# Performance work log

Measured on AMD Instinct MI355X. Metric: run time of the kernel, lower is better.

The kernel has to match this reference:

```python
import jax, jax.numpy as jnp
import numpy as np

N_NODES = 100_000
N_EDGES = 1_600_000
N_GRAPHS = 1024
IN_CH = 5
EPS_BN = 1e-5


def _p(key, shape, scale=0.1):
    return scale * jax.random.normal(key, shape, dtype=jnp.float32)


def setup_inputs() -> dict:
    key = jax.random.key(0)
    ks = jax.random.split(key, 24)
    x = jax.random.normal(ks[0], (N_NODES, IN_CH), dtype=jnp.float32)
    edge_index = jax.random.randint(ks[1], (2, N_EDGES), 0, N_NODES, dtype=jnp.int64)
    batch = jnp.sort(jax.random.randint(ks[2], (N_NODES,), 0, N_GRAPHS, dtype=jnp.int64))
    return {
        "x": x, "edge_index": edge_index, "batch": batch,
        "W1": _p(ks[3], (IN_CH, 128)), "a1_src": _p(ks[4], (4, 32)), "a1_dst": _p(ks[5], (4, 32)), "b1": jnp.zeros((128,), jnp.float32),
        "g1": jnp.ones((128,), jnp.float32), "be1": jnp.zeros((128,), jnp.float32),
        "W2": _p(ks[6], (128, 128)), "a2_src": _p(ks[7], (4, 32)), "a2_dst": _p(ks[8], (4, 32)), "b2": jnp.zeros((128,), jnp.float32),
        "g2": jnp.ones((128,), jnp.float32), "be2": jnp.zeros((128,), jnp.float32),
        # conv3: 128 -> 64, 1 head, mean (concat=False)
        "W3": _p(ks[9], (128, 64)), "a3_src": _p(ks[10], (1, 64)), "a3_dst": _p(ks[11], (1, 64)), "b3": jnp.zeros((64,), jnp.float32),
        # classifier Linear(128,64) -> ELU -> Linear(64,1)
        "fc1_w": _p(ks[12], (128, 64)), "fc1_b": jnp.zeros((64,), jnp.float32),
        "fc2_w": _p(ks[13], (64, 1)), "fc2_b": jnp.zeros((1,), jnp.float32),
    }


def _gat_conv(x, src, dst, W, a_src, a_dst, bias, heads, out_ch, concat):
    """PyG GATConv (negative_slope=0.2, self-loops already appended, eval-mode dropout)."""
    n = x.shape[0]
    h = (x @ W).reshape(n, heads, out_ch)                      # [N,H,C]
    al_s = jnp.sum(h * a_src, axis=-1)                         # [N,H]
    al_d = jnp.sum(h * a_dst, axis=-1)                         # [N,H]
    e = jax.nn.leaky_relu(al_s[src] + al_d[dst], 0.2)          # [E,H]
    m = jax.lax.stop_gradient(jax.ops.segment_max(e, dst, num_segments=n))
    p = jnp.exp(e - m[dst])
    s = jax.ops.segment_sum(p, dst, num_segments=n)
    alpha = p / (s[dst] + 1e-16)                               # segment softmax over in-edges of dst
    out = jax.ops.segment_sum(h[src] * alpha[:, :, None], dst, num_segments=n)  # [N,H,C]
    out = out.reshape(n, heads * out_ch) if concat else out.mean(axis=1)
    return out + bias


def _bn(x, g, b):
    mu = x.mean(axis=0)
    var = x.var(axis=0)
    return (x - mu) * jax.lax.rsqrt(var + EPS_BN) * g + b


def reference(x, edge_index, batch,
              W1, a1_src, a1_dst, b1, g1, be1,
              W2, a2_src, a2_dst, b2, g2, be2,
              W3, a3_src, a3_dst, b3,
              fc1_w, fc1_b, fc2_w, fc2_b):
    n = x.shape[0]
    # PyG GATConv default add_self_loops=True
    loops = jnp.arange(n, dtype=edge_index.dtype)
    src = jnp.concatenate([edge_index[0], loops])
    dst = jnp.concatenate([edge_index[1], loops])

    h = jax.nn.elu(_bn(_gat_conv(x, src, dst, W1, a1_src, a1_dst, b1, 4, 32, True), g1, be1))
    h = jax.nn.elu(_bn(_gat_conv(h, src, dst, W2, a2_src, a2_dst, b2, 4, 32, True), g2, be2))
    h = jax.nn.elu(_gat_conv(h, src, dst, W3, a3_src, a3_dst, b3, 1, 64, False))  # [N,64]

    counts = jax.ops.segment_sum(jnp.ones((n,), h.dtype), batch, num_segments=N_GRAPHS)
    mean_p = jax.ops.segment_sum(h, batch, num_segments=N_GRAPHS) / jnp.maximum(counts, 1.0)[:, None]
    max_p = jax.ops.segment_max(h, batch, num_segments=N_GRAPHS)
    max_p = jnp.where(counts[:, None] > 0, max_p, 0.0)
    hg = jnp.concatenate([mean_p, max_p], axis=1)              # [B,128]

    z = jax.nn.elu(hg @ fc1_w + fc1_b)
    return (z @ fc2_w + fc2_b).squeeze(-1)                     # [B]
```

## Files before the change

### kernel.cpp

```cpp
#include <hip/hip_runtime.h>
#include <hip/hip_bf16.h>


#define BSHIFT 7
#define BCAP 4096
#define SCH 32

typedef __attribute__((ext_vector_type(8))) short short8;
typedef __attribute__((ext_vector_type(4))) float f32x4;

__device__ __forceinline__ float leaky02(float e) { return e > 0.f ? e : 0.2f * e; }

__device__ __forceinline__ unsigned short bf16u(float x) {
    __hip_bfloat16 b = __float2bfloat16(x);
    return *(unsigned short*)&b;
}
__device__ __forceinline__ unsigned pack_bf2(float a, float b) {
    return (unsigned)bf16u(a) | ((unsigned)bf16u(b) << 16);
}
__device__ __forceinline__ float bf_lo(unsigned u) { return __uint_as_float(u << 16); }
__device__ __forceinline__ float bf_hi(unsigned u) { return __uint_as_float(u & 0xffff0000u); }

__global__ __launch_bounds__(256) void k_bhist(const int* __restrict__ dst,
                                               int* __restrict__ bcount, int E, int nb) {
    __shared__ int hist[1024];
    for (int i = threadIdx.x; i < nb; i += 256) hist[i] = 0;
    __syncthreads();
    for (int i = blockIdx.x * blockDim.x + threadIdx.x; i < E; i += gridDim.x * blockDim.x)
        atomicAdd(&hist[dst[i] >> BSHIFT], 1);
    __syncthreads();
    for (int i = threadIdx.x; i < nb; i += 256) {
        int c = hist[i];
        if (c) atomicAdd(&bcount[i], c);
    }
}

__global__ __launch_bounds__(1024) void k_bscan(const int* __restrict__ bcount,
                                                int* __restrict__ bucketPtr,
                                                int* __restrict__ cursor,
                                                int* __restrict__ rowPtr, int nb, int N) {
    __shared__ int sh[1024];
    int tid = threadIdx.x;
    int v = (tid < nb) ? bcount[tid] : 0;
    sh[tid] = v;
    __syncthreads();
#pragma unroll
    for (int off = 1; off < 1024; off <<= 1) {
        int t = (tid >= off) ? sh[tid - off] : 0;
        __syncthreads();
        sh[tid] += t;
        __syncthreads();
    }
    if (tid < nb) {
        int ex = sh[tid] - v;
        bucketPtr[tid] = ex;
        cursor[tid] = ex;
    }
    if (tid == nb - 1) {
        bucketPtr[nb] = sh[tid];
        rowPtr[N] = sh[tid];
    }
}

__global__ __launch_bounds__(256) void k_bscatter(const int* __restrict__ src,
                                                  const int* __restrict__ dst,
                                                  int* __restrict__ cursor,
                                                  uint2* __restrict__ ebuf, int E, int nb) {
    __shared__ int hist[1024];
    __shared__ int baseArr[1024];
    int tid = threadIdx.x;
    int chunk0 = blockIdx.x * (256 * SCH);
    for (int i = tid; i < nb; i += 256) hist[i] = 0;
    __syncthreads();
    int rank[SCH];
#pragma unroll
    for (int it = 0; it < SCH; it++) {
        int e = chunk0 + it * 256 + tid;
        rank[it] = (e < E) ? atomicAdd(&hist[dst[e] >> BSHIFT], 1) : 0;
    }
    __syncthreads();
    for (int b = tid; b < nb; b += 256) {
        int c = hist[b];
        baseArr[b] = c ? atomicAdd(&cursor[b], c) : 0;
    }
    __syncthreads();
#pragma unroll
    for (int it = 0; it < SCH; it++) {
        int e = chunk0 + it * 256 + tid;
        if (e < E) {
            int d = dst[e];
            int pos = baseArr[d >> BSHIFT] + rank[it];
            ebuf[pos] = make_uint2((unsigned)d, (unsigned)src[e]);
        }
    }
}

__global__ __launch_bounds__(256) void k_bsort(const uint2* __restrict__ ebuf,
                                               const int* __restrict__ bucketPtr,
                                               int* __restrict__ rowPtr,
                                               int* __restrict__ colv, int N) {
    int b = blockIdx.x;
    int base = bucketPtr[b], end = bucketPtr[b + 1];
    int count = end - base;
    int tid = threadIdx.x;
    __shared__ int hist[128], scanin[128], hist2[128];
    __shared__ int lrank[BCAP];
    __shared__ int lsrc[BCAP];
    if (tid < 128) { hist[tid] = 0; hist2[tid] = 0; }
    __syncthreads();
    bool staged = (count <= BCAP);
    for (int i = tid; i < count; i += 256) {
        uint2 p = ebuf[base + i];
        int local = p.x & 127;
        int r = atomicAdd(&hist[local], 1);
        if (staged) lrank[i] = (r << 7) | local;
    }
    __syncthreads();
    if (tid < 128) scanin[tid] = hist[tid];
    __syncthreads();
#pragma unroll
    for (int off = 1; off < 128; off <<= 1) {
        int v = 0;
        if (tid < 128 && tid >= off) v = scanin[tid - off];
        __syncthreads();
        if (tid < 128) scanin[tid] += v;
        __syncthreads();
    }
    int nodeBase = b << BSHIFT;
    if (tid < 128) {
        int n = nodeBase + tid;
        if (n < N) rowPtr[n] = base + scanin[tid] - hist[tid];
    }
    __syncthreads();
    if (staged) {
        for (int i = tid; i < count; i += 256) {
            uint2 p = ebuf[base + i];
            int lr = lrank[i];
            int local = lr & 127;
            int pos = (scanin[local] - hist[local]) + (lr >> 7);
            lsrc[pos] = (int)p.y;
        }
        __syncthreads();
        for (int i = tid; i < count; i += 256) colv[base + i] = lsrc[i];
    } else {
        for (int i = tid; i < count; i += 256) {
            uint2 p = ebuf[base + i];
            int local = p.x & 127;
            int r = atomicAdd(&hist2[local], 1);
            colv[base + (scanin[local] - hist[local]) + r] = (int)p.y;
        }
    }
}

__global__ __launch_bounds__(256) void k_l1(const float* __restrict__ x, const float* __restrict__ W,
                                            const float* __restrict__ asrc, const float* __restrict__ adst,
                                            unsigned* __restrict__ hb, float* __restrict__ als,
                                            float* __restrict__ ald, int N) {
    int w = (blockIdx.x * blockDim.x + threadIdx.x) >> 6;
    if (w >= N) return;
    int lane = threadIdx.x & 63;
    float xv[5];
#pragma unroll
    for (int k = 0; k < 5; k++) xv[k] = x[(size_t)w * 5 + k];
    int c0 = 2 * lane;
    float h0 = 0.f, h1 = 0.f;
#pragma unroll
    for (int k = 0; k < 5; k++) {
        float2 wv = ((const float2*)(W + k * 128))[lane];
        h0 += xv[k] * wv.x;
        h1 += xv[k] * wv.y;
    }
    hb[(size_t)w * 64 + lane] = pack_bf2(h0, h1);
    float s = h0 * asrc[c0] + h1 * asrc[c0 + 1];
    float d = h0 * adst[c0] + h1 * adst[c0 + 1];
#pragma unroll
    for (int off = 1; off <= 8; off <<= 1) { s += __shfl_xor(s, off); d += __shfl_xor(d, off); }
    if ((lane & 15) == 0) {
        int g = lane >> 4;
        als[(size_t)w * 4 + g] = s;
        ald[(size_t)w * 4 + g] = d;
    }
}

__global__ __launch_bounds__(256) void k_agg128(const unsigned* __restrict__ h,
                                                const float* __restrict__ als, const float* __restrict__ ald,
                                                const int* __restrict__ rowPtr, const int* __restrict__ colv,
                                                const float* __restrict__ bias,
                                                float* __restrict__ out, int N) {
    int w = (blockIdx.x * blockDim.x + threadIdx.x) >> 6;
    if (w >= N) return;
    int lane = threadIdx.x & 63;
    int grp = lane >> 4;
    int l16 = lane & 15;
    int head = l16 >> 2;
    float aldn = ald[(size_t)w * 4 + head];
    float acc[8] = {};
    float dsum = 0.f;

    auto edge = [&](int s) {
        float a = als[(size_t)s * 4 + head];
        float wt = __expf(leaky02(a + aldn));
        uint4 u = *(const uint4*)&h[(size_t)s * 64 + l16 * 4];
        acc[0] += wt * bf_lo(u.x); acc[1] += wt * bf_hi(u.x);
        acc[2] += wt * bf_lo(u.y); acc[3] += wt * bf_hi(u.y);
        acc[4] += wt * bf_lo(u.z); acc[5] += wt * bf_hi(u.z);
        acc[6] += wt * bf_lo(u.w); acc[7] += wt * bf_hi(u.w);
        dsum += wt;
    };

    if (grp == 0) edge(w);
    int beg = rowPtr[w], end = rowPtr[w + 1];
    int p = beg + grp;
    for (; p + 12 < end; p += 16) {
        int s0 = colv[p], s1 = colv[p + 4], s2 = colv[p + 8], s3 = colv[p + 12];
        float a0 = als[(size_t)s0 * 4 + head];
        float a1 = als[(size_t)s1 * 4 + head];
        float a2 = als[(size_t)s2 * 4 + head];
        float a3 = als[(size_t)s3 * 4 + head];
        uint4 u0 = *(const uint4*)&h[(size_t)s0 * 64 + l16 * 4];
        uint4 u1 = *(const uint4*)&h[(size_t)s1 * 64 + l16 * 4];
        uint4 u2 = *(const uint4*)&h[(size_t)s2 * 64 + l16 * 4];
        uint4 u3 = *(const uint4*)&h[(size_t)s3 * 64 + l16 * 4];
        float w0 = __expf(leaky02(a0 + aldn));
        float w1 = __expf(leaky02(a1 + aldn));
        float w2 = __expf(leaky02(a2 + aldn));
        float w3 = __expf(leaky02(a3 + aldn));
        acc[0] += w0 * bf_lo(u0.x) + w1 * bf_lo(u1.x) + w2 * bf_lo(u2.x) + w3 * bf_lo(u3.x);
        acc[1] += w0 * bf_hi(u0.x) + w1 * bf_hi(u1.x) + w2 * bf_hi(u2.x) + w3 * bf_hi(u3.x);
        acc[2] += w0 * bf_lo(u0.y) + w1 * bf_lo(u1.y) + w2 * bf_lo(u2.y) + w3 * bf_lo(u3.y);
        acc[3] += w0 * bf_hi(u0.y) + w1 * bf_hi(u1.y) + w2 * bf_hi(u2.y) + w3 * bf_hi(u3.y);
        acc[4] += w0 * bf_lo(u0.z) + w1 * bf_lo(u1.z) + w2 * bf_lo(u2.z) + w3 * bf_lo(u3.z);
        acc[5] += w0 * bf_hi(u0.z) + w1 * bf_hi(u1.z) + w2 * bf_hi(u2.z) + w3 * bf_hi(u3.z);
        acc[6] += w0 * bf_lo(u0.w) + w1 * bf_lo(u1.w) + w2 * bf_lo(u2.w) + w3 * bf_lo(u3.w);
        acc[7] += w0 * bf_hi(u0.w) + w1 * bf_hi(u1.w) + w2 * bf_hi(u2.w) + w3 * bf_hi(u3.w);
        dsum += w0 + w1 + w2 + w3;
    }
    for (; p < end; p += 4) edge(colv[p]);

#pragma unroll
    for (int i = 0; i < 8; i++) {
        acc[i] += __shfl_xor(acc[i], 16);
        acc[i] += __shfl_xor(acc[i], 32);
    }
    dsum += __shfl_xor(dsum, 16);
    dsum += __shfl_xor(dsum, 32);

    if (grp == 0) {
        float inv = 1.f / (dsum + 1e-16f);
        const float4* b4 = (const float4*)(bias + 8 * l16);
        float4 bv0 = b4[0], bv1 = b4[1];
        float4 o0, o1;
        o0.x = acc[0] * inv + bv0.x; o0.y = acc[1] * inv + bv0.y;
        o0.z = acc[2] * inv + bv0.z; o0.w = acc[3] * inv + bv0.w;
        o1.x = acc[4] * inv + bv1.x; o1.y = acc[5] * inv + bv1.y;
        o1.z = acc[6] * inv + bv1.z; o1.w = acc[7] * inv + bv1.w;
        float4* op = (float4*)(out + (size_t)w * 128 + 8 * l16);
        op[0] = o0;
        op[1] = o1;
    }
}

__global__ __launch_bounds__(256) void k_agg64(const unsigned* __restrict__ h,
                                               const float* __restrict__ als, const float* __restrict__ ald,
                                               const int* __restrict__ rowPtr, const int* __restrict__ colv,
                                               const float* __restrict__ bias,
                                               float* __restrict__ out, int N) {
    int w = (blockIdx.x * blockDim.x + threadIdx.x) >> 6;
    if (w >= N) return;
    int lane = threadIdx.x & 63;
    int grp = lane >> 3;
    int l8 = lane & 7;
    float aldn = ald[w];
    float acc[8] = {};
    float dsum = 0.f;

    auto edge = [&](int s) {
        float wt = __expf(leaky02(als[s] + aldn));
        uint4 u = *(const uint4*)&h[(size_t)s * 32 + l8 * 4];
        acc[0] += wt * bf_lo(u.x); acc[1] += wt * bf_hi(u.x);
        acc[2] += wt * bf_lo(u.y); acc[3] += wt * bf_hi(u.y);
        acc[4] += wt * bf_lo(u.z); acc[5] += wt * bf_hi(u.z);
        acc[6] += wt * bf_lo(u.w); acc[7] += wt * bf_hi(u.w);
        dsum += wt;
    };

    if (grp == 0) edge(w);
    int beg = rowPtr[w], end = rowPtr[w + 1];
    int p = beg + grp;
    for (; p + 8 < end; p += 16) {
        int s0 = colv[p], s1 = colv[p + 8];
        float a0 = als[s0], a1 = als[s1];
        uint4 u0 = *(const uint4*)&h[(size_t)s0 * 32 + l8 * 4];
        uint4 u1 = *(const uint4*)&h[(size_t)s1 * 32 + l8 * 4];
        float w0 = __expf(leaky02(a0 + aldn));
        float w1 = __expf(leaky02(a1 + aldn));
        acc[0] += w0 * bf_lo(u0.x) + w1 * bf_lo(u1.x);
        acc[1] += w0 * bf_hi(u0.x) + w1 * bf_hi(u1.x);
        acc[2] += w0 * bf_lo(u0.y) + w1 * bf_lo(u1.y);
        acc[3] += w0 * bf_hi(u0.y) + w1 * bf_hi(u1.y);
        acc[4] += w0 * bf_lo(u0.z) + w1 * bf_lo(u1.z);
        acc[5] += w0 * bf_hi(u0.z) + w1 * bf_hi(u1.z);
        acc[6] += w0 * bf_lo(u0.w) + w1 * bf_lo(u1.w);
        acc[7] += w0 * bf_hi(u0.w) + w1 * bf_hi(u1.w);
        dsum += w0 + w1;
    }
    if (p < end) edge(colv[p]);

#pragma unroll
    for (int i = 0; i < 8; i++) {
        acc[i] += __shfl_xor(acc[i], 8);
        acc[i] += __shfl_xor(acc[i], 16);
        acc[i] += __shfl_xor(acc[i], 32);
    }
    dsum += __shfl_xor(dsum, 8);
    dsum += __shfl_xor(dsum, 16);
    dsum += __shfl_xor(dsum, 32);

    if (grp == 0) {
        float inv = 1.f / (dsum + 1e-16f);
        const float4* b4 = (const float4*)(bias + 8 * l8);
        float4 bv0 = b4[0], bv1 = b4[1];
        float v[8];
#pragma unroll
        for (int i = 0; i < 8; i++) v[i] = acc[i] * inv;
        v[0] += bv0.x; v[1] += bv0.y; v[2] += bv0.z; v[3] += bv0.w;
        v[4] += bv1.x; v[5] += bv1.y; v[6] += bv1.z; v[7] += bv1.w;
#pragma unroll
        for (int i = 0; i < 8; i++) v[i] = v[i] > 0.f ? v[i] : expm1f(v[i]);
        float4* op = (float4*)(out + (size_t)w * 64 + 8 * l8);
        op[0] = make_float4(v[0], v[1], v[2], v[3]);
        op[1] = make_float4(v[4], v[5], v[6], v[7]);
    }
}

__global__ __launch_bounds__(256) void k_bnstats(const float* __restrict__ x,
                                                 float* __restrict__ stats, int N) {
    int tid = threadIdx.x;
    int c = tid & 127;
    int half = tid >> 7;
    float s = 0.f, q = 0.f;
    for (int r = blockIdx.x * 2 + half; r < N; r += gridDim.x * 2) {
        float v = x[(size_t)r * 128 + c];
        s += v;
        q += v * v;
    }
    __shared__ float ls[256], lq[256];
    ls[tid] = s; lq[tid] = q;
    __syncthreads();
    if (tid < 128) {
        atomicAdd(&stats[c], ls[tid] + ls[tid + 128]);
        atomicAdd(&stats[128 + c], lq[tid] + lq[tid + 128]);
    }
}

template <int BN>
__global__ __launch_bounds__(256) void k_gemm_mfma(
        const float* __restrict__ A, const float* __restrict__ W,
        const float* __restrict__ stats, const float* __restrict__ g,
        const float* __restrict__ be,
        unsigned* __restrict__ hb, float* __restrict__ als, float* __restrict__ ald,
        const float* __restrict__ asrc, const float* __restrict__ adst,
        int M, float invN) {
    constexpr int NT = BN / 16;
    __shared__ unsigned short Wt[BN][136];
    __shared__ unsigned short At[64][136];
    __shared__ float sc[128], sh[128];
    const int tid = threadIdx.x;
    const int wave = tid >> 6, lane = tid & 63;
    const int quad = lane >> 4, l16 = lane & 15;
    const int r0 = blockIdx.x * 64;

    if (tid < 128) {
        float mean = stats[tid] * invN;
        float var = stats[128 + tid] * invN - mean * mean;
        float s = rsqrtf(var + 1e-5f) * g[tid];
        sc[tid] = s;
        sh[tid] = be[tid] - mean * s;
    }
    for (int i = tid; i < 128 * (BN / 4); i += 256) {
        int k = i / (BN / 4);
        int n4 = (i % (BN / 4)) * 4;
        float4 v = *(const float4*)(W + (size_t)k * BN + n4);
        Wt[n4 + 0][k] = bf16u(v.x);
        Wt[n4 + 1][k] = bf16u(v.y);
        Wt[n4 + 2][k] = bf16u(v.z);
        Wt[n4 + 3][k] = bf16u(v.w);
    }
    __syncthreads();
    for (int i = tid; i < 64 * 32; i += 256) {
        int row = i >> 5;
        int c4 = (i & 31) << 2;
        int r = r0 + row;
        float4 v = make_float4(0.f, 0.f, 0.f, 0.f);
        if (r < M) v = *(const float4*)(A + (size_t)r * 128 + c4);
        float t0 = v.x * sc[c4 + 0] + sh[c4 + 0];
        float t1 = v.y * sc[c4 + 1] + sh[c4 + 1];
        float t2 = v.z * sc[c4 + 2] + sh[c4 + 2];
        float t3 = v.w * sc[c4 + 3] + sh[c4 + 3];
        t0 = t0 > 0.f ? t0 : expm1f(t0);
        t1 = t1 > 0.f ? t1 : expm1f(t1);
        t2 = t2 > 0.f ? t2 : expm1f(t2);
        t3 = t3 > 0.f ? t3 : expm1f(t3);
        unsigned u0 = (unsigned)bf16u(t0) | ((unsigned)bf16u(t1) << 16);
        unsigned u1 = (unsigned)bf16u(t2) | ((unsigned)bf16u(t3) << 16);
        *(uint2*)&At[row][c4] = make_uint2(u0, u1);
    }
    __syncthreads();

    short8 afr[4];
#pragma unroll
    for (int ks = 0; ks < 4; ks++)
        afr[ks] = *(const short8*)&At[wave * 16 + l16][ks * 32 + quad * 8];
    f32x4 acc[NT];
#pragma unroll
    for (int nt = 0; nt < NT; nt++) acc[nt] = (f32x4){0.f, 0.f, 0.f, 0.f};
#pragma unroll
    for (int ks = 0; ks < 4; ks++) {
#pragma unroll
        for (int nt = 0; nt < NT; nt++) {
            short8 bfrag = *(const short8*)&Wt[nt * 16 + l16][ks * 32 + quad * 8];
            acc[nt] = __builtin_amdgcn_mfma_f32_16x16x32_bf16(afr[ks], bfrag, acc[nt], 0, 0, 0);
        }
    }

    float as_[NT], ad_[NT];
#pragma unroll
    for (int nt = 0; nt < NT; nt++) {
        as_[nt] = asrc[nt * 16 + l16];
        ad_[nt] = adst[nt * 16 + l16];
    }

#pragma unroll
    for (int r = 0; r < 4; r++) {
        int gr = r0 + wave * 16 + quad * 4 + r;
        if constexpr (BN == 128) {
            float sv[4] = {0.f, 0.f, 0.f, 0.f}, dv[4] = {0.f, 0.f, 0.f, 0.f};
#pragma unroll
            for (int nt = 0; nt < NT; nt++) {
                float v = acc[nt][r];
                sv[nt >> 1] += v * as_[nt];
                dv[nt >> 1] += v * ad_[nt];
            }
#pragma unroll
            for (int hd = 0; hd < 4; hd++) {
                float s = sv[hd], d = dv[hd];
                s += __shfl_xor(s, 1); s += __shfl_xor(s, 2);
                s += __shfl_xor(s, 4); s += __shfl_xor(s, 8);
                d += __shfl_xor(d, 1); d += __shfl_xor(d, 2);
                d += __shfl_xor(d, 4); d += __shfl_xor(d, 8);
                if (l16 == 0 && gr < M) {
                    als[(size_t)gr * 4 + hd] = s;
                    ald[(size_t)gr * 4 + hd] = d;
                }
            }
        } else {
            float s = 0.f, d = 0.f;
#pragma unroll
            for (int nt = 0; nt < NT; nt++) {
                float v = acc[nt][r];
                s += v * as_[nt];
                d += v * ad_[nt];
            }
            s += __shfl_xor(s, 1); s += __shfl_xor(s, 2);
            s += __shfl_xor(s, 4); s += __shfl_xor(s, 8);
            d += __shfl_xor(d, 1); d += __shfl_xor(d, 2);
            d += __shfl_xor(d, 4); d += __shfl_xor(d, 8);
            if (l16 == 0 && gr < M) { als[gr] = s; ald[gr] = d; }
        }
    }
#pragma unroll
    for (int nt = 0; nt < NT; nt++) {
#pragma unroll
        for (int r = 0; r < 4; r++) {
            float v = acc[nt][r];
            float o = __shfl_xor(v, 1);
            if ((lane & 1) == 0) {
                int gr = r0 + wave * 16 + quad * 4 + r;
                if (gr < M)
                    hb[(size_t)gr * (BN / 2) + nt * 8 + (l16 >> 1)] = pack_bf2(v, o);
            }
        }
    }
}

__global__ __launch_bounds__(64) void k_pool(const float* __restrict__ h, const int* __restrict__ batch,
                                             const float* __restrict__ fc1w, const float* __restrict__ fc1b,
                                             const float* __restrict__ fc2w, const float* __restrict__ fc2b,
                                             float* __restrict__ out, int N) {
    int g = blockIdx.x;
    int lane = threadIdx.x;
    int lo, hi;
    {
        int a = 0, b = N;
        while (a < b) { int m = (a + b) >> 1; if (batch[m] < g) a = m + 1; else b = m; }
        lo = a;
    }
    {
        int a = lo, b = N;
        while (a < b) { int m = (a + b) >> 1; if (batch[m] < g + 1) a = m + 1; else b = m; }
        hi = a;
    }
    float sum = 0.f, mx = -3.4e38f;
    for (int r = lo; r < hi; r++) {
        float v = h[(size_t)r * 64 + lane];
        sum += v;
        mx = fmaxf(mx, v);
    }
    int cnt = hi - lo;
    float mean = sum / fmaxf((float)cnt, 1.f);
    if (cnt == 0) mx = 0.f;
    __shared__ float hg[128];
    hg[lane] = mean;
    hg[64 + lane] = mx;
    __syncthreads();
    float z = fc1b[lane];
    for (int k = 0; k < 128; k++) z += hg[k] * fc1w[k * 64 + lane];
    z = z > 0.f ? z : expm1f(z);
    float o = z * fc2w[lane];
#pragma unroll
    for (int off = 32; off >= 1; off >>= 1) o += __shfl_down(o, off);
    if (lane == 0) out[g] = o + fc2b[0];
}

extern "C" void kernel_launch(void* const* d_in, const int* in_sizes, int n_in,
                              void* d_out, int out_size, void* d_ws, size_t ws_size,
                              hipStream_t stream) {
    const float* x = (const float*)d_in[0];
    const int* ei = (const int*)d_in[1];
    const int* batch = (const int*)d_in[2];
    const float* W1 = (const float*)d_in[3];
    const float* a1s = (const float*)d_in[4];
    const float* a1d = (const float*)d_in[5];
    const float* b1 = (const float*)d_in[6];
    const float* g1 = (const float*)d_in[7];
    const float* be1 = (const float*)d_in[8];
    const float* W2 = (const float*)d_in[9];
    const float* a2s = (const float*)d_in[10];
    const float* a2d = (const float*)d_in[11];
    const float* b2 = (const float*)d_in[12];
    const float* g2 = (const float*)d_in[13];
    const float* be2 = (const float*)d_in[14];
    const float* W3 = (const float*)d_in[15];
    const float* a3s = (const float*)d_in[16];
    const float* a3d = (const float*)d_in[17];
    const float* b3 = (const float*)d_in[18];
    const float* fc1w = (const float*)d_in[19];
    const float* fc1b = (const float*)d_in[20];
    const float* fc2w = (const float*)d_in[21];
    const float* fc2b = (const float*)d_in[22];

    const int N = in_sizes[2];
    const int E = in_sizes[1] / 2;
    const int NG = out_size;
    const int* src = ei;
    const int* dst = ei + E;
    const int nb = (N + 127) >> BSHIFT;

    char* ws = (char*)d_ws;
    size_t off = 0;
    auto alloc = [&](size_t bytes) -> void* {
        void* p = ws + off;
        off += (bytes + 255) / 256 * 256;
        return p;
    };
    float* bufA = (float*)alloc((size_t)N * 128 * 4);
    unsigned* hb = (unsigned*)alloc((size_t)N * 64 * 4);
    float* h3 = (float*)alloc((size_t)N * 64 * 4);
    int* colArr = (int*)alloc((size_t)E * 4);
    int* rowPtr = (int*)alloc((size_t)(N + 1) * 4);
    int* bcount = (int*)alloc((size_t)nb * 4);
    int* bucketPtr = (int*)alloc((size_t)(nb + 1) * 4);
    int* cursor = (int*)alloc((size_t)nb * 4);
    float* als = (float*)alloc((size_t)N * 4 * 4);
    float* ald = (float*)alloc((size_t)N * 4 * 4);
    float* stats = (float*)alloc(512 * 4);
    uint2* ebuf = (uint2*)h3;

    hipMemsetAsync(bcount, 0, (size_t)nb * 4, stream);
    hipMemsetAsync(stats, 0, 512 * 4, stream);

    const int waveBlocks = (N * 64 + 255) / 256;
    const int gemmBlocks = (N + 63) / 64;
    const float invN = 1.f / N;

    k_bhist<<<256, 256, 0, stream>>>(dst, bcount, E, nb);
    k_bscan<<<1, 1024, 0, stream>>>(bcount, bucketPtr, cursor, rowPtr, nb, N);
    k_bscatter<<<(E + 256 * SCH - 1) / (256 * SCH), 256, 0, stream>>>(src, dst, cursor, ebuf, E, nb);
    k_bsort<<<nb, 256, 0, stream>>>(ebuf, bucketPtr, rowPtr, colArr, N);

    k_l1<<<waveBlocks, 256, 0, stream>>>(x, W1, a1s, a1d, hb, als, ald, N);
    k_agg128<<<waveBlocks, 256, 0, stream>>>(hb, als, ald, rowPtr, colArr, b1, bufA, N);
    k_bnstats<<<512, 256, 0, stream>>>(bufA, stats, N);

    k_gemm_mfma<128><<<gemmBlocks, 256, 0, stream>>>(bufA, W2, stats, g1, be1,
                                                     hb, als, ald, a2s, a2d, N, invN);
    k_agg128<<<waveBlocks, 256, 0, stream>>>(hb, als, ald, rowPtr, colArr, b2, bufA, N);
    k_bnstats<<<512, 256, 0, stream>>>(bufA, stats + 256, N);

    k_gemm_mfma<64><<<gemmBlocks, 256, 0, stream>>>(bufA, W3, stats + 256, g2, be2,
                                                    hb, als, ald, a3s, a3d, N, invN);
    k_agg64<<<waveBlocks, 256, 0, stream>>>(hb, als, ald, rowPtr, colArr, b3, h3, N);

    k_pool<<<NG, 64, 0, stream>>>(h3, batch, fc1w, fc1b, fc2w, fc2b, (float*)d_out, N);
}
```

Measured before the change: 608.6 us.

## Store aggregation outputs in bf16 and simplify edge loops

```diff
diff --git a/kernel.cpp b/kernel.cpp
--- a/kernel.cpp
+++ b/kernel.cpp
@@ -186,7 +186,7 @@
                                                 const float* __restrict__ als, const float* __restrict__ ald,
                                                 const int* __restrict__ rowPtr, const int* __restrict__ colv,
                                                 const float* __restrict__ bias,
-                                                float* __restrict__ out, int N) {
+                                                unsigned* __restrict__ out, int N) {
     int w = (blockIdx.x * blockDim.x + threadIdx.x) >> 6;
     if (w >= N) return;
     int lane = threadIdx.x & 63;
@@ -211,31 +211,12 @@
     if (grp == 0) edge(w);
     int beg = rowPtr[w], end = rowPtr[w + 1];
     int p = beg + grp;
-    for (; p + 12 < end; p += 16) {
-        int s0 = colv[p], s1 = colv[p + 4], s2 = colv[p + 8], s3 = colv[p + 12];
-        float a0 = als[(size_t)s0 * 4 + head];
-        float a1 = als[(size_t)s1 * 4 + head];
-        float a2 = als[(size_t)s2 * 4 + head];
-        float a3 = als[(size_t)s3 * 4 + head];
-        uint4 u0 = *(const uint4*)&h[(size_t)s0 * 64 + l16 * 4];
-        uint4 u1 = *(const uint4*)&h[(size_t)s1 * 64 + l16 * 4];
-        uint4 u2 = *(const uint4*)&h[(size_t)s2 * 64 + l16 * 4];
-        uint4 u3 = *(const uint4*)&h[(size_t)s3 * 64 + l16 * 4];
-        float w0 = __expf(leaky02(a0 + aldn));
-        float w1 = __expf(leaky02(a1 + aldn));
-        float w2 = __expf(leaky02(a2 + aldn));
-        float w3 = __expf(leaky02(a3 + aldn));
-        acc[0] += w0 * bf_lo(u0.x) + w1 * bf_lo(u1.x) + w2 * bf_lo(u2.x) + w3 * bf_lo(u3.x);
-        acc[1] += w0 * bf_hi(u0.x) + w1 * bf_hi(u1.x) + w2 * bf_hi(u2.x) + w3 * bf_hi(u3.x);
-        acc[2] += w0 * bf_lo(u0.y) + w1 * bf_lo(u1.y) + w2 * bf_lo(u2.y) + w3 * bf_lo(u3.y);
-        acc[3] += w0 * bf_hi(u0.y) + w1 * bf_hi(u1.y) + w2 * bf_hi(u2.y) + w3 * bf_hi(u3.y);
-        acc[4] += w0 * bf_lo(u0.z) + w1 * bf_lo(u1.z) + w2 * bf_lo(u2.z) + w3 * bf_lo(u3.z);
-        acc[5] += w0 * bf_hi(u0.z) + w1 * bf_hi(u1.z) + w2 * bf_hi(u2.z) + w3 * bf_hi(u3.z);
-        acc[6] += w0 * bf_lo(u0.w) + w1 * bf_lo(u1.w) + w2 * bf_lo(u2.w) + w3 * bf_lo(u3.w);
-        acc[7] += w0 * bf_hi(u0.w) + w1 * bf_hi(u1.w) + w2 * bf_hi(u2.w) + w3 * bf_hi(u3.w);
-        dsum += w0 + w1 + w2 + w3;
-    }
-    for (; p < end; p += 4) edge(colv[p]);
+    for (; p + 4 < end; p += 8) {
+        int s0 = colv[p], s1 = colv[p + 4];
+        edge(s0);
+        edge(s1);
+    }
+    if (p < end) edge(colv[p]);
 
 #pragma unroll
     for (int i = 0; i < 8; i++) {
@@ -249,14 +230,17 @@
         float inv = 1.f / (dsum + 1e-16f);
         const float4* b4 = (const float4*)(bias + 8 * l16);
         float4 bv0 = b4[0], bv1 = b4[1];
-        float4 o0, o1;
-        o0.x = acc[0] * inv + bv0.x; o0.y = acc[1] * inv + bv0.y;
-        o0.z = acc[2] * inv + bv0.z; o0.w = acc[3] * inv + bv0.w;
-        o1.x = acc[4] * inv + bv1.x; o1.y = acc[5] * inv + bv1.y;
-        o1.z = acc[6] * inv + bv1.z; o1.w = acc[7] * inv + bv1.w;
-        float4* op = (float4*)(out + (size_t)w * 128 + 8 * l16);
-        op[0] = o0;
-        op[1] = o1;
+        float v[8];
+        v[0] = acc[0] * inv + bv0.x; v[1] = acc[1] * inv + bv0.y;
+        v[2] = acc[2] * inv + bv0.z; v[3] = acc[3] * inv + bv0.w;
+        v[4] = acc[4] * inv + bv1.x; v[5] = acc[5] * inv + bv1.y;
+        v[6] = acc[6] * inv + bv1.z; v[7] = acc[7] * inv + bv1.w;
+        uint4 o;
+        o.x = pack_bf2(v[0], v[1]);
+        o.y = pack_bf2(v[2], v[3]);
+        o.z = pack_bf2(v[4], v[5]);
+        o.w = pack_bf2(v[6], v[7]);
+        *(uint4*)&out[(size_t)w * 64 + l16 * 4] = o;
     }
 }
 
@@ -264,7 +248,7 @@
                                                const float* __restrict__ als, const float* __restrict__ ald,
                                                const int* __restrict__ rowPtr, const int* __restrict__ colv,
                                                const float* __restrict__ bias,
-                                               float* __restrict__ out, int N) {
+                                               unsigned* __restrict__ out, int N) {
     int w = (blockIdx.x * blockDim.x + threadIdx.x) >> 6;
     if (w >= N) return;
     int lane = threadIdx.x & 63;
@@ -289,20 +273,8 @@
     int p = beg + grp;
     for (; p + 8 < end; p += 16) {
         int s0 = colv[p], s1 = colv[p + 8];
-        float a0 = als[s0], a1 = als[s1];
-        uint4 u0 = *(const uint4*)&h[(size_t)s0 * 32 + l8 * 4];
-        uint4 u1 = *(const uint4*)&h[(size_t)s1 * 32 + l8 * 4];
-        float w0 = __expf(leaky02(a0 + aldn));
-        float w1 = __expf(leaky02(a1 + aldn));
-        acc[0] += w0 * bf_lo(u0.x) + w1 * bf_lo(u1.x);
-        acc[1] += w0 * bf_hi(u0.x) + w1 * bf_hi(u1.x);
-        acc[2] += w0 * bf_lo(u0.y) + w1 * bf_lo(u1.y);
-        acc[3] += w0 * bf_hi(u0.y) + w1 * bf_hi(u1.y);
-        acc[4] += w0 * bf_lo(u0.z) + w1 * bf_lo(u1.z);
-        acc[5] += w0 * bf_hi(u0.z) + w1 * bf_hi(u1.z);
-        acc[6] += w0 * bf_lo(u0.w) + w1 * bf_lo(u1.w);
-        acc[7] += w0 * bf_hi(u0.w) + w1 * bf_hi(u1.w);
-        dsum += w0 + w1;
+        edge(s0);
+        edge(s1);
     }
     if (p < end) edge(colv[p]);
 
@@ -327,35 +299,44 @@
         v[4] += bv1.x; v[5] += bv1.y; v[6] += bv1.z; v[7] += bv1.w;
 #pragma unroll
         for (int i = 0; i < 8; i++) v[i] = v[i] > 0.f ? v[i] : expm1f(v[i]);
-        float4* op = (float4*)(out + (size_t)w * 64 + 8 * l8);
-        op[0] = make_float4(v[0], v[1], v[2], v[3]);
-        op[1] = make_float4(v[4], v[5], v[6], v[7]);
-    }
-}
-
-__global__ __launch_bounds__(256) void k_bnstats(const float* __restrict__ x,
-                                                 float* __restrict__ stats, int N) {
+        uint4 o;
+        o.x = pack_bf2(v[0], v[1]);
+        o.y = pack_bf2(v[2], v[3]);
+        o.z = pack_bf2(v[4], v[5]);
+        o.w = pack_bf2(v[6], v[7]);
+        *(uint4*)&out[(size_t)w * 32 + l8 * 4] = o;
+    }
+}
+
+__global__ __launch_bounds__(256) void k_bnstats_b(const unsigned* __restrict__ x,
+                                                   float* __restrict__ stats, int N) {
+    __shared__ float lsum[128], lsq[128];
     int tid = threadIdx.x;
-    int c = tid & 127;
-    int half = tid >> 7;
-    float s = 0.f, q = 0.f;
-    for (int r = blockIdx.x * 2 + half; r < N; r += gridDim.x * 2) {
-        float v = x[(size_t)r * 128 + c];
-        s += v;
-        q += v * v;
-    }
-    __shared__ float ls[256], lq[256];
-    ls[tid] = s; lq[tid] = q;
+    if (tid < 128) { lsum[tid] = 0.f; lsq[tid] = 0.f; }
+    __syncthreads();
+    int wrd = tid & 63;
+    int part = tid >> 6;
+    float s0 = 0.f, q0 = 0.f, s1 = 0.f, q1 = 0.f;
+    for (int r = blockIdx.x * 4 + part; r < N; r += gridDim.x * 4) {
+        unsigned u = x[(size_t)r * 64 + wrd];
+        float a = bf_lo(u), b = bf_hi(u);
+        s0 += a; q0 += a * a;
+        s1 += b; q1 += b * b;
+    }
+    atomicAdd(&lsum[2 * wrd], s0);
+    atomicAdd(&lsum[2 * wrd + 1], s1);
+    atomicAdd(&lsq[2 * wrd], q0);
+    atomicAdd(&lsq[2 * wrd + 1], q1);
     __syncthreads();
     if (tid < 128) {
-        atomicAdd(&stats[c], ls[tid] + ls[tid + 128]);
-        atomicAdd(&stats[128 + c], lq[tid] + lq[tid + 128]);
+        atomicAdd(&stats[tid], lsum[tid]);
+        atomicAdd(&stats[128 + tid], lsq[tid]);
     }
 }
 
 template <int BN>
 __global__ __launch_bounds__(256) void k_gemm_mfma(
-        const float* __restrict__ A, const float* __restrict__ W,
+        const unsigned* __restrict__ A, const float* __restrict__ W,
         const float* __restrict__ stats, const float* __restrict__ g,
         const float* __restrict__ be,
         unsigned* __restrict__ hb, float* __restrict__ als, float* __restrict__ ald,
@@ -389,21 +370,22 @@
     __syncthreads();
     for (int i = tid; i < 64 * 32; i += 256) {
         int row = i >> 5;
-        int c4 = (i & 31) << 2;
+        int p2 = i & 31;
+        int c = p2 * 4;
         int r = r0 + row;
-        float4 v = make_float4(0.f, 0.f, 0.f, 0.f);
-        if (r < M) v = *(const float4*)(A + (size_t)r * 128 + c4);
-        float t0 = v.x * sc[c4 + 0] + sh[c4 + 0];
-        float t1 = v.y * sc[c4 + 1] + sh[c4 + 1];
-        float t2 = v.z * sc[c4 + 2] + sh[c4 + 2];
-        float t3 = v.w * sc[c4 + 3] + sh[c4 + 3];
+        uint2 v = make_uint2(0u, 0u);
+        if (r < M) v = *(const uint2*)(A + (size_t)r * 64 + p2 * 2);
+        float t0 = bf_lo(v.x) * sc[c + 0] + sh[c + 0];
+        float t1 = bf_hi(v.x) * sc[c + 1] + sh[c + 1];
+        float t2 = bf_lo(v.y) * sc[c + 2] + sh[c + 2];
+        float t3 = bf_hi(v.y) * sc[c + 3] + sh[c + 3];
         t0 = t0 > 0.f ? t0 : expm1f(t0);
         t1 = t1 > 0.f ? t1 : expm1f(t1);
         t2 = t2 > 0.f ? t2 : expm1f(t2);
         t3 = t3 > 0.f ? t3 : expm1f(t3);
-        unsigned u0 = (unsigned)bf16u(t0) | ((unsigned)bf16u(t1) << 16);
-        unsigned u1 = (unsigned)bf16u(t2) | ((unsigned)bf16u(t3) << 16);
-        *(uint2*)&At[row][c4] = make_uint2(u0, u1);
+        unsigned u0 = pack_bf2(t0, t1);
+        unsigned u1 = pack_bf2(t2, t3);
+        *(uint2*)&At[row][c] = make_uint2(u0, u1);
     }
     __syncthreads();
 
@@ -483,7 +465,7 @@
     }
 }
 
-__global__ __launch_bounds__(64) void k_pool(const float* __restrict__ h, const int* __restrict__ batch,
+__global__ __launch_bounds__(64) void k_pool(const unsigned* __restrict__ h, const int* __restrict__ batch,
                                              const float* __restrict__ fc1w, const float* __restrict__ fc1b,
                                              const float* __restrict__ fc2w, const float* __restrict__ fc2b,
                                              float* __restrict__ out, int N) {
@@ -500,18 +482,27 @@
         while (a < b) { int m = (a + b) >> 1; if (batch[m] < g + 1) a = m + 1; else b = m; }
         hi = a;
     }
-    float sum = 0.f, mx = -3.4e38f;
-    for (int r = lo; r < hi; r++) {
-        float v = h[(size_t)r * 64 + lane];
-        sum += v;
-        mx = fmaxf(mx, v);
-    }
+    int wrd = lane & 31, half = lane >> 5;
+    float s0 = 0.f, s1 = 0.f, m0 = -3.4e38f, m1 = -3.4e38f;
+    for (int r = lo + half; r < hi; r += 2) {
+        unsigned u = h[(size_t)r * 32 + wrd];
+        float a = bf_lo(u), b = bf_hi(u);
+        s0 += a; s1 += b;
+        m0 = fmaxf(m0, a); m1 = fmaxf(m1, b);
+    }
+    s0 += __shfl_xor(s0, 32);
+    s1 += __shfl_xor(s1, 32);
+    m0 = fmaxf(m0, __shfl_xor(m0, 32));
+    m1 = fmaxf(m1, __shfl_xor(m1, 32));
     int cnt = hi - lo;
-    float mean = sum / fmaxf((float)cnt, 1.f);
-    if (cnt == 0) mx = 0.f;
     __shared__ float hg[128];
-    hg[lane] = mean;
-    hg[64 + lane] = mx;
+    if (half == 0) {
+        float invc = 1.f / fmaxf((float)cnt, 1.f);
+        hg[2 * wrd] = s0 * invc;
+        hg[2 * wrd + 1] = s1 * invc;
+        hg[64 + 2 * wrd] = (cnt > 0) ? m0 : 0.f;
+        hg[64 + 2 * wrd + 1] = (cnt > 0) ? m1 : 0.f;
+    }
     __syncthreads();
     float z = fc1b[lane];
     for (int k = 0; k < 128; k++) z += hg[k] * fc1w[k * 64 + lane];
@@ -563,9 +554,10 @@
         off += (bytes + 255) / 256 * 256;
         return p;
     };
-    float* bufA = (float*)alloc((size_t)N * 128 * 4);
+    unsigned* bufAb = (unsigned*)alloc((size_t)N * 64 * 4);
     unsigned* hb = (unsigned*)alloc((size_t)N * 64 * 4);
-    float* h3 = (float*)alloc((size_t)N * 64 * 4);
+    unsigned* h3b = (unsigned*)alloc((size_t)N * 32 * 4);
+    float* ebufF = (float*)alloc((size_t)E * 8);
     int* colArr = (int*)alloc((size_t)E * 4);
     int* rowPtr = (int*)alloc((size_t)(N + 1) * 4);
     int* bcount = (int*)alloc((size_t)nb * 4);
@@ -574,7 +566,7 @@
     float* als = (float*)alloc((size_t)N * 4 * 4);
     float* ald = (float*)alloc((size_t)N * 4 * 4);
     float* stats = (float*)alloc(512 * 4);
-    uint2* ebuf = (uint2*)h3;
+    uint2* ebuf = (uint2*)ebufF;
 
     hipMemsetAsync(bcount, 0, (size_t)nb * 4, stream);
     hipMemsetAsync(stats, 0, 512 * 4, stream);
@@ -589,17 +581,17 @@
     k_bsort<<<nb, 256, 0, stream>>>(ebuf, bucketPtr, rowPtr, colArr, N);
 
     k_l1<<<waveBlocks, 256, 0, stream>>>(x, W1, a1s, a1d, hb, als, ald, N);
-    k_agg128<<<waveBlocks, 256, 0, stream>>>(hb, als, ald, rowPtr, colArr, b1, bufA, N);
-    k_bnstats<<<512, 256, 0, stream>>>(bufA, stats, N);
-
-    k_gemm_mfma<128><<<gemmBlocks, 256, 0, stream>>>(bufA, W2, stats, g1, be1,
+    k_agg128<<<waveBlocks, 256, 0, stream>>>(hb, als, ald, rowPtr, colArr, b1, bufAb, N);
+    k_bnstats_b<<<512, 256, 0, stream>>>(bufAb, stats, N);
+
+    k_gemm_mfma<128><<<gemmBlocks, 256, 0, stream>>>(bufAb, W2, stats, g1, be1,
                                                      hb, als, ald, a2s, a2d, N, invN);
-    k_agg128<<<waveBlocks, 256, 0, stream>>>(hb, als, ald, rowPtr, colArr, b2, bufA, N);
-    k_bnstats<<<512, 256, 0, stream>>>(bufA, stats + 256, N);
-
-    k_gemm_mfma<64><<<gemmBlocks, 256, 0, stream>>>(bufA, W3, stats + 256, g2, be2,
+    k_agg128<<<waveBlocks, 256, 0, stream>>>(hb, als, ald, rowPtr, colArr, b2, bufAb, N);
+    k_bnstats_b<<<512, 256, 0, stream>>>(bufAb, stats + 256, N);
+
+    k_gemm_mfma<64><<<gemmBlocks, 256, 0, stream>>>(bufAb, W3, stats + 256, g2, be2,
                                                     hb, als, ald, a3s, a3d, N, invN);
-    k_agg64<<<waveBlocks, 256, 0, stream>>>(hb, als, ald, rowPtr, colArr, b3, h3, N);
-
-    k_pool<<<NG, 64, 0, stream>>>(h3, batch, fc1w, fc1b, fc2w, fc2b, (float*)d_out, N);
-}
+    k_agg64<<<waveBlocks, 256, 0, stream>>>(hb, als, ald, rowPtr, colArr, b3, h3b, N);
+
+    k_pool<<<NG, 64, 0, stream>>>(h3b, batch, fc1w, fc1b, fc2w, fc2b, (float*)d_out, N);
+}
```

After: 555.0 us. 8.8% less time.
